# Kernel tuning notes

Hardware: AMD Instinct MI355X
Metric: run time of the kernel (lower is better)

The kernel has to match this reference:

```python
import jax, jax.numpy as jnp
import numpy as np

N_NODES = 50000
N_EDGES = 1600000
IN_DIM, HID, HEADS, OUT_DIM = 128, 32, 4, 16
NEG_SLOPE = 0.2  # DGL GATConv default


def setup_inputs() -> dict:
    key = jax.random.key(0)
    ks = jax.random.split(key, 12)
    features = jax.random.normal(ks[0], (N_NODES, IN_DIM), dtype=jnp.float32)
    src = jax.random.randint(ks[1], (N_EDGES,), 0, N_NODES, dtype=jnp.int32)
    dst = jax.random.randint(ks[2], (N_EDGES,), 0, N_NODES, dtype=jnp.int32)
    # layer 1 params (xavier-style scale)
    W1 = jax.random.normal(ks[3], (IN_DIM, HEADS * HID), dtype=jnp.float32) * (2.0 / (IN_DIM + HEADS * HID)) ** 0.5
    al1 = jax.random.normal(ks[4], (HEADS, HID), dtype=jnp.float32) * 0.1
    ar1 = jax.random.normal(ks[5], (HEADS, HID), dtype=jnp.float32) * 0.1
    b1 = jnp.zeros((HEADS * HID,), dtype=jnp.float32)
    # layer 2 params
    W2 = jax.random.normal(ks[6], (HID, OUT_DIM), dtype=jnp.float32) * (2.0 / (HID + OUT_DIM)) ** 0.5
    al2 = jax.random.normal(ks[7], (1, OUT_DIM), dtype=jnp.float32) * 0.1
    ar2 = jax.random.normal(ks[8], (1, OUT_DIM), dtype=jnp.float32) * 0.1
    b2 = jnp.zeros((OUT_DIM,), dtype=jnp.float32)
    return {"features": features, "src": src, "dst": dst,
            "W1": W1, "al1": al1, "ar1": ar1, "b1": b1,
            "W2": W2, "al2": al2, "ar2": ar2, "b2": b2}


def gat_conv(x, src, dst, W, al, ar, b, n_nodes):
    """DGL GATConv (no dropout, no residual). Returns [N, H, out]."""
    H, out = al.shape
    feat = (x @ W).reshape(-1, H, out)                       # [N,H,out]
    el = jnp.sum(feat * al, axis=-1)                         # [N,H]
    er = jnp.sum(feat * ar, axis=-1)                         # [N,H]
    e = jax.nn.leaky_relu(el[src] + er[dst], NEG_SLOPE)      # [E,H]
    # segment softmax over incoming edges per destination node
    m = jax.ops.segment_max(e, dst, num_segments=n_nodes)    # [N,H]
    ex = jnp.exp(e - m[dst])                                 # [E,H]
    s = jax.ops.segment_sum(ex, dst, num_segments=n_nodes)   # [N,H]
    alpha = ex / s[dst]                                      # [E,H]
    msg = alpha[:, :, None] * feat[src]                      # [E,H,out]
    rst = jax.ops.segment_sum(msg, dst, num_segments=n_nodes)
    return rst + b.reshape(H, out)


def reference(features, src, dst, W1, al1, ar1, b1, W2, al2, ar2, b2):
    n = features.shape[0]
    x1 = gat_conv(features, src, dst, W1, al1, ar1, b1, n)   # [N,HEADS,HID]
    x1 = jnp.mean(jax.nn.relu(x1), axis=1)                   # [N,HID]
    x2 = gat_conv(x1, src, dst, W2, al2, ar2, b2, n)         # [N,1,OUT]
    x2 = jnp.squeeze(x2, axis=1)                             # [N,OUT]
    return jax.nn.log_softmax(x2, axis=-1)
```

## Files before the change

### kernel.cpp

```cpp
#include <hip/hip_runtime.h>
#include <math.h>

#define NEG_SLOPE 0.2f
#define BINCAP 10240

typedef __attribute__((ext_vector_type(8))) short short8;
typedef __attribute__((ext_vector_type(4))) float f32x4;

__device__ __forceinline__ float lrelu(float x) {
    return x >= 0.f ? x : NEG_SLOPE * x;
}
__device__ __forceinline__ unsigned bf16_rne(float f) {
    unsigned b = __float_as_uint(f);
    return (b + 0x7FFFu + ((b >> 16) & 1u)) >> 16;
}

__global__ __launch_bounds__(256) void init_cursor(int* __restrict__ bin_cursor) {
    bin_cursor[threadIdx.x] = threadIdx.x * BINCAP;
}

__global__ __launch_bounds__(256) void scatter_bins(
    const int* __restrict__ src, const int* __restrict__ dst,
    int* __restrict__ bin_cursor, unsigned* __restrict__ binned,
    int E, int nbins)
{
    __shared__ int hist[256];
    __shared__ int base_l[256];
    int tid = threadIdx.x;
    hist[tid] = 0;
    __syncthreads();
    int epb = (E + gridDim.x - 1) / gridDim.x;
    int beg = blockIdx.x * epb, end = min(E, beg + epb);
    for (int e = beg + tid; e < end; e += 256)
        atomicAdd(&hist[dst[e] >> 8], 1);
    __syncthreads();
    if (tid < nbins) {
        int c = hist[tid];
        base_l[tid] = (c > 0) ? atomicAdd(&bin_cursor[tid], c) : 0;
    }
    __syncthreads();
    hist[tid] = 0;
    __syncthreads();
    for (int e = beg + tid; e < end; e += 256) {
        int d = dst[e];
        int bin = d >> 8;
        int slot = atomicAdd(&hist[bin], 1);
        binned[base_l[bin] + slot] = ((unsigned)(d & 255) << 16) | (unsigned)src[e];
    }
}

__global__ __launch_bounds__(256) void local_sort(
    const unsigned* __restrict__ binned, const int* __restrict__ bin_cursor,
    int* __restrict__ rowptr, unsigned short* __restrict__ deg,
    unsigned short* __restrict__ csr, int N, int nbins)
{
    __shared__ int cnt[256];
    __shared__ int sh[256];
    int b = blockIdx.x;
    int t = threadIdx.x;
    int gbase = b * BINCAP;
    int gcount = bin_cursor[b] - gbase;
    cnt[t] = 0;
    __syncthreads();
    for (int i = t; i < gcount; i += 256)
        atomicAdd(&cnt[binned[gbase + i] >> 16], 1);
    __syncthreads();
    int own = cnt[t];
    sh[t] = own;
    __syncthreads();
#pragma unroll
    for (int off = 1; off < 256; off <<= 1) {
        int v = (t >= off) ? sh[t - off] : 0;
        __syncthreads();
        sh[t] += v;
        __syncthreads();
    }
    int excl = sh[t] - own;
    int dcount = min(256, N - (b << 8));
    if (t < dcount) {
        rowptr[(b << 8) + t] = gbase + excl;
        deg[(b << 8) + t] = (unsigned short)own;
    }
    cnt[t] = excl;
    __syncthreads();
    for (int i = t; i < gcount; i += 256) {
        unsigned w = binned[gbase + i];
        int slot = atomicAdd(&cnt[w >> 16], 1);
        csr[gbase + slot] = (unsigned short)(w & 0xFFFFu);
    }
}

__global__ __launch_bounds__(256) void convert_w1(
    const float* __restrict__ W, unsigned short* __restrict__ Wt)
{
    int i = blockIdx.x * 256 + threadIdx.x;
    int kin = i >> 7, nout = i & 127;
    Wt[nout * 128 + kin] = (unsigned short)bf16_rne(W[kin * 128 + nout]);
}

__global__ __launch_bounds__(256) void gemm1_mfma(
    const float* __restrict__ X, const unsigned short* __restrict__ Wt,
    unsigned short* __restrict__ feat1b, int N)
{
    __shared__ unsigned short Xb[64][136];
    __shared__ unsigned short Wb[128][136];
    int tid = threadIdx.x;
    int nb = blockIdx.x * 64;

    for (int idx = tid; idx < 128 * 16; idx += 256) {
        int row = idx >> 4, q = idx & 15;
        *(uint4*)&Wb[row][q * 8] = *(const uint4*)&Wt[row * 128 + q * 8];
    }
    for (int idx = tid; idx < 64 * 32; idx += 256) {
        int row = idx >> 5, q = idx & 31;
        int n = nb + row;
        float4 v = (n < N) ? *(const float4*)&X[(size_t)n * 128 + q * 4]
                           : make_float4(0.f, 0.f, 0.f, 0.f);
        unsigned lo = bf16_rne(v.x) | (bf16_rne(v.y) << 16);
        unsigned hi = bf16_rne(v.z) | (bf16_rne(v.w) << 16);
        *(uint2*)&Xb[row][q * 4] = make_uint2(lo, hi);
    }
    __syncthreads();

    int wave = tid >> 6, lane = tid & 63;
    int m = lane & 15, quad = lane >> 4;
    f32x4 acc[8];
#pragma unroll
    for (int t = 0; t < 8; ++t) acc[t] = (f32x4){0.f, 0.f, 0.f, 0.f};

#pragma unroll
    for (int kt = 0; kt < 4; ++kt) {
        int k0 = kt * 32 + quad * 8;
        short8 a = *(const short8*)&Xb[wave * 16 + m][k0];
#pragma unroll
        for (int t = 0; t < 8; ++t) {
            short8 b = *(const short8*)&Wb[t * 16 + m][k0];
            acc[t] = __builtin_amdgcn_mfma_f32_16x16x32_bf16(a, b, acc[t], 0, 0, 0);
        }
    }

#pragma unroll
    for (int r = 0; r < 4; ++r) {
        int n = nb + wave * 16 + quad * 4 + r;
        if (n < N) {
#pragma unroll
            for (int t = 0; t < 8; ++t)
                feat1b[(size_t)n * 128 + t * 16 + m] =
                    (unsigned short)bf16_rne(acc[t][r]);
        }
    }
}

__global__ __launch_bounds__(256) void el_er1(
    const unsigned short* __restrict__ feat1b, const float* __restrict__ al,
    const float* __restrict__ ar, float* __restrict__ el1,
    float* __restrict__ er1, int N)
{
    int t = blockIdx.x * 256 + threadIdx.x;
    if (t >= N * 4) return;
    int n = t >> 2, h = t & 3;
    const unsigned* fp = (const unsigned*)(feat1b + (size_t)n * 128 + h * 32);
    const float* alh = al + h * 32;
    const float* arh = ar + h * 32;
    float pel = 0.f, per = 0.f;
#pragma unroll
    for (int q = 0; q < 16; ++q) {
        unsigned u = fp[q];
        float f0 = __uint_as_float(u << 16);
        float f1 = __uint_as_float(u & 0xFFFF0000u);
        pel += f0 * alh[2 * q] + f1 * alh[2 * q + 1];
        per += f0 * arh[2 * q] + f1 * arh[2 * q + 1];
    }
    el1[t] = pel;
    er1[t] = per;
}

__global__ __launch_bounds__(256) void agg1_fused(
    const int* __restrict__ rowptr, const unsigned short* __restrict__ deg,
    const unsigned short* __restrict__ csr,
    const unsigned short* __restrict__ feat1b, const float* __restrict__ el1,
    const float* __restrict__ er1, const float* __restrict__ b1,
    const float* __restrict__ W2, const float* __restrict__ al2,
    const float* __restrict__ ar2, unsigned short* __restrict__ feat2b,
    float* __restrict__ el2, float* __restrict__ er2, int N)
{
    __shared__ uint2 pairs[4][4][66];
    int gid = blockIdx.x * 256 + threadIdx.x;
    int d = gid >> 6;
    if (d >= N) return;
    int wv = (threadIdx.x >> 6) & 3;
    int lane = threadIdx.x & 63;
    int h = lane >> 4;
    float4 er4 = ((const float4*)er1)[d];
    int beg = rowptr[d], end = beg + (int)deg[d];
    const unsigned* feat32 = (const unsigned*)feat1b;

    float M = -INFINITY, S = 0.f, a0 = 0.f, a1 = 0.f;

    for (int base = beg; base < end; base += 64) {
        int cnt = min(64, end - base);
        int sn = 0;
        float4 v = make_float4(-INFINITY, -INFINITY, -INFINITY, -INFINITY);
        if (lane < cnt) {
            sn = (int)csr[base + lane];
            float4 el4 = ((const float4*)el1)[sn];
            v.x = lrelu(el4.x + er4.x);
            v.y = lrelu(el4.y + er4.y);
            v.z = lrelu(el4.z + er4.z);
            v.w = lrelu(el4.w + er4.w);
        }
        float4 cm = v;
#pragma unroll
        for (int off = 1; off < 64; off <<= 1) {
            cm.x = fmaxf(cm.x, __shfl_xor(cm.x, off));
            cm.y = fmaxf(cm.y, __shfl_xor(cm.y, off));
            cm.z = fmaxf(cm.z, __shfl_xor(cm.z, off));
            cm.w = fmaxf(cm.w, __shfl_xor(cm.w, off));
        }
        float4 w;
        w.x = __expf(v.x - cm.x);
        w.y = __expf(v.y - cm.y);
        w.z = __expf(v.z - cm.z);
        w.w = __expf(v.w - cm.w);
        unsigned snb = (unsigned)sn << 6;
        pairs[wv][0][lane] = make_uint2(snb, __float_as_uint(w.x));
        pairs[wv][1][lane] = make_uint2(snb, __float_as_uint(w.y));
        pairs[wv][2][lane] = make_uint2(snb, __float_as_uint(w.z));
        pairs[wv][3][lane] = make_uint2(snb, __float_as_uint(w.w));

        float cmh = (h & 2) ? ((h & 1) ? cm.w : cm.z) : ((h & 1) ? cm.y : cm.x);
        float nM = fmaxf(M, cmh);
        float so = __expf(M - nM);
        float sc = __expf(cmh - nM);
        M = nM;

        float ca0 = 0.f, ca1 = 0.f, cs = 0.f;
        for (int i = 0; i < cnt; ++i) {
            uint2 p = pairs[wv][h][i];
            float wb = __uint_as_float(p.y);
            unsigned u = feat32[p.x + lane];
            float f0 = __uint_as_float(u << 16);
            float f1 = __uint_as_float(u & 0xFFFF0000u);
            ca0 += wb * f0;
            ca1 += wb * f1;
            cs += wb;
        }
        S = S * so + cs * sc;
        a0 = a0 * so + ca0 * sc;
        a1 = a1 * so + ca1 * sc;
    }
    float inv = (end > beg) ? (1.f / S) : 0.f;
    float o0 = a0 * inv, o1 = a1 * inv;

    int dim0 = lane * 2;
    float2 bb = *(const float2*)(b1 + dim0);
    float r0 = fmaxf(o0 + bb.x, 0.f);
    float r1 = fmaxf(o1 + bb.y, 0.f);
    r0 += __shfl_xor(r0, 16); r0 += __shfl_xor(r0, 32);
    r1 += __shfl_xor(r1, 16); r1 += __shfl_xor(r1, 32);
    float u0 = 0.25f * r0;
    float u1 = 0.25f * r1;

    int j = lane & 15;
    float f2 = 0.f;
#pragma unroll
    for (int i = 0; i < 16; ++i) {
        float xa = __shfl(u0, i);
        float xb = __shfl(u1, i);
        f2 += xa * W2[(2 * i) * 16 + j] + xb * W2[(2 * i + 1) * 16 + j];
    }
    float pel = f2 * al2[j], per = f2 * ar2[j];
#pragma unroll
    for (int off = 1; off < 16; off <<= 1) {
        pel += __shfl_xor(pel, off);
        per += __shfl_xor(per, off);
    }
    if (lane < 16) feat2b[(size_t)d * 16 + j] = (unsigned short)bf16_rne(f2);
    if (lane == 0) { el2[d] = pel; er2[d] = per; }
}

__global__ __launch_bounds__(256) void agg2_fused(
    const int* __restrict__ rowptr, const unsigned short* __restrict__ deg,
    const unsigned short* __restrict__ csr,
    const unsigned short* __restrict__ feat2b, const float* __restrict__ el2,
    const float* __restrict__ er2, const float* __restrict__ b2,
    float* __restrict__ out, int N)
{
    __shared__ uint2 pairs2[4][4][18];
    int gid = blockIdx.x * 256 + threadIdx.x;
    int d = gid >> 4;
    if (d >= N) return;
    int tid = threadIdx.x;
    int wv = (tid >> 6) & 3;
    int grp = (tid >> 4) & 3;
    int l16 = tid & 15;
    float er = er2[d];
    int beg = rowptr[d], end = beg + (int)deg[d];

    float M = -INFINITY, S = 0.f, a = 0.f;
    for (int cb = beg; cb < end; cb += 16) {
        int cnt = min(16, end - cb);
        int sn = 0;
        float v = -INFINITY;
        if (l16 < cnt) {
            sn = (int)csr[cb + l16];
            v = lrelu(el2[sn] + er);
        }
        float cm = v;
#pragma unroll
        for (int off = 1; off < 16; off <<= 1)
            cm = fmaxf(cm, __shfl_xor(cm, off));
        float w = __expf(v - cm);
        pairs2[wv][grp][l16] = make_uint2((unsigned)sn << 4, __float_as_uint(w));
        float nM = fmaxf(M, cm);
        float so = __expf(M - nM);
        float sc = __expf(cm - nM);
        M = nM;
        float ca = 0.f, cs = 0.f;
        for (int i = 0; i < cnt; ++i) {
            uint2 p = pairs2[wv][grp][i];
            float wb = __uint_as_float(p.y);
            unsigned u = (unsigned)feat2b[p.x + l16];
            float f = __uint_as_float(u << 16);
            ca += wb * f;
            cs += wb;
        }
        S = S * so + cs * sc;
        a = a * so + ca * sc;
    }
    float inv = (end > beg) ? (1.f / S) : 0.f;
    float val = a * inv + b2[l16];
    float mm = val;
#pragma unroll
    for (int off = 1; off < 16; off <<= 1)
        mm = fmaxf(mm, __shfl_xor(mm, off));
    float ex = __expf(val - mm);
    float ssum = ex;
#pragma unroll
    for (int off = 1; off < 16; off <<= 1)
        ssum += __shfl_xor(ssum, off);
    out[(size_t)d * 16 + l16] = val - (mm + __logf(ssum));
}

extern "C" void kernel_launch(void* const* d_in, const int* in_sizes, int n_in,
                              void* d_out, int out_size, void* d_ws, size_t ws_size,
                              hipStream_t stream)
{
    const float* X   = (const float*)d_in[0];
    const int*   src = (const int*)d_in[1];
    const int*   dst = (const int*)d_in[2];
    const float* W1  = (const float*)d_in[3];
    const float* al1 = (const float*)d_in[4];
    const float* ar1 = (const float*)d_in[5];
    const float* b1  = (const float*)d_in[6];
    const float* W2  = (const float*)d_in[7];
    const float* al2 = (const float*)d_in[8];
    const float* ar2 = (const float*)d_in[9];
    const float* b2  = (const float*)d_in[10];
    int N = in_sizes[0] / 128;
    int E = in_sizes[1];
    int nbins = (N + 255) >> 8;

    float* ws = (float*)d_ws;
    size_t o = 0;
    unsigned short* feat1b = (unsigned short*)(ws + o); o += (size_t)N * 64;
    float* el1   = ws + o; o += (size_t)N * 4;
    float* er1   = ws + o; o += (size_t)N * 4;
    unsigned short* feat2b = (unsigned short*)(ws + o); o += (size_t)N * 8;
    float* el2   = ws + o; o += (size_t)N;
    float* er2   = ws + o; o += (size_t)N;
    int* rowptr  = (int*)(ws + o); o += (size_t)N;
    unsigned short* deg = (unsigned short*)(ws + o); o += (size_t)N / 2 + 1;
    unsigned short* Wt1b = (unsigned short*)(ws + o); o += 128 * 128 / 2;
    int* bin_cursor = (int*)(ws + o); o += 256;
    unsigned* binned = (unsigned*)(ws + o); o += (size_t)nbins * BINCAP;
    unsigned short* csr = (unsigned short*)(ws + o); o += (size_t)nbins * BINCAP / 2 + 1;
    float* out = (float*)d_out;

    init_cursor<<<1, 256, 0, stream>>>(bin_cursor);
    scatter_bins<<<256, 256, 0, stream>>>(src, dst, bin_cursor, binned, E, nbins);
    local_sort<<<nbins, 256, 0, stream>>>(binned, bin_cursor, rowptr, deg, csr, N, nbins);

    convert_w1<<<64, 256, 0, stream>>>(W1, Wt1b);
    gemm1_mfma<<<(N + 63) / 64, 256, 0, stream>>>(X, Wt1b, feat1b, N);
    el_er1<<<(N * 4 + 255) / 256, 256, 0, stream>>>(feat1b, al1, ar1, el1, er1, N);

    agg1_fused<<<(N * 64 + 255) / 256, 256, 0, stream>>>(
        rowptr, deg, csr, feat1b, el1, er1, b1, W2, al2, ar2, feat2b, el2, er2, N);

    agg2_fused<<<(N * 16 + 255) / 256, 256, 0, stream>>>(
        rowptr, deg, csr, feat2b, el2, er2, b2, out, N);
}
```

Before: 250.9 us.

## Fuse prep kernels, stage edges in LDS, fuse el/er into GEMM, widen agg2

Merges init_cursor and convert_w1 into a single prep launch, and fuses the el/er attention-logit computation into the MFMA GEMM epilogue using shuffle reductions, which removes a pass over feat1b. scatter_bins now runs with 512 blocks and stages packed (dst,src) words in shared memory, so dst and src are read from global memory only once. agg2 moves from 16 lanes per node to a full 64-lane wave that splits edges across four sub-groups and then reduces, and agg1's accumulators use float2 vectors. The trade-offs are more shared memory per scatter block, less precise el/er (computed from fp32 accumulators instead of rounded bf16), and wasted lanes in agg2 for low-degree nodes.

Result: no change. 251.0 us (+0.1%).

```diff
diff --git a/kernel.cpp b/kernel.cpp
--- a/kernel.cpp
+++ b/kernel.cpp
@@ -6,6 +6,7 @@
 
 typedef __attribute__((ext_vector_type(8))) short short8;
 typedef __attribute__((ext_vector_type(4))) float f32x4;
+typedef __attribute__((ext_vector_type(2))) float f32x2;
 
 __device__ __forceinline__ float lrelu(float x) {
     return x >= 0.f ? x : NEG_SLOPE * x;
@@ -15,8 +16,17 @@
     return (b + 0x7FFFu + ((b >> 16) & 1u)) >> 16;
 }
 
-__global__ __launch_bounds__(256) void init_cursor(int* __restrict__ bin_cursor) {
-    bin_cursor[threadIdx.x] = threadIdx.x * BINCAP;
+__global__ __launch_bounds__(256) void prep(
+    const float* __restrict__ W, unsigned short* __restrict__ Wt,
+    int* __restrict__ bin_cursor)
+{
+    if (blockIdx.x == 64) {
+        bin_cursor[threadIdx.x] = threadIdx.x * BINCAP;
+        return;
+    }
+    int i = blockIdx.x * 256 + threadIdx.x;
+    int kin = i >> 7, nout = i & 127;
+    Wt[nout * 128 + kin] = (unsigned short)bf16_rne(W[kin * 128 + nout]);
 }
 
 __global__ __launch_bounds__(256) void scatter_bins(
@@ -24,6 +34,7 @@
     int* __restrict__ bin_cursor, unsigned* __restrict__ binned,
     int E, int nbins)
 {
+    __shared__ unsigned stage[3328];
     __shared__ int hist[256];
     __shared__ int base_l[256];
     int tid = threadIdx.x;
@@ -31,8 +42,12 @@
     __syncthreads();
     int epb = (E + gridDim.x - 1) / gridDim.x;
     int beg = blockIdx.x * epb, end = min(E, beg + epb);
-    for (int e = beg + tid; e < end; e += 256)
-        atomicAdd(&hist[dst[e] >> 8], 1);
+    int cnt_local = end - beg;
+    for (int k = tid; k < cnt_local; k += 256) {
+        int d = dst[beg + k];
+        stage[k] = ((unsigned)d << 16) | (unsigned)src[beg + k];
+        atomicAdd(&hist[d >> 8], 1);
+    }
     __syncthreads();
     if (tid < nbins) {
         int c = hist[tid];
@@ -41,11 +56,11 @@
     __syncthreads();
     hist[tid] = 0;
     __syncthreads();
-    for (int e = beg + tid; e < end; e += 256) {
-        int d = dst[e];
-        int bin = d >> 8;
+    for (int k = tid; k < cnt_local; k += 256) {
+        unsigned w = stage[k];
+        int bin = w >> 24;
         int slot = atomicAdd(&hist[bin], 1);
-        binned[base_l[bin] + slot] = ((unsigned)(d & 255) << 16) | (unsigned)src[e];
+        binned[base_l[bin] + slot] = w;
     }
 }
 
@@ -63,7 +78,7 @@
     cnt[t] = 0;
     __syncthreads();
     for (int i = t; i < gcount; i += 256)
-        atomicAdd(&cnt[binned[gbase + i] >> 16], 1);
+        atomicAdd(&cnt[(binned[gbase + i] >> 16) & 255], 1);
     __syncthreads();
     int own = cnt[t];
     sh[t] = own;
@@ -85,22 +100,16 @@
     __syncthreads();
     for (int i = t; i < gcount; i += 256) {
         unsigned w = binned[gbase + i];
-        int slot = atomicAdd(&cnt[w >> 16], 1);
+        int slot = atomicAdd(&cnt[(w >> 16) & 255], 1);
         csr[gbase + slot] = (unsigned short)(w & 0xFFFFu);
     }
-}
-
-__global__ __launch_bounds__(256) void convert_w1(
-    const float* __restrict__ W, unsigned short* __restrict__ Wt)
-{
-    int i = blockIdx.x * 256 + threadIdx.x;
-    int kin = i >> 7, nout = i & 127;
-    Wt[nout * 128 + kin] = (unsigned short)bf16_rne(W[kin * 128 + nout]);
 }
 
 __global__ __launch_bounds__(256) void gemm1_mfma(
     const float* __restrict__ X, const unsigned short* __restrict__ Wt,
-    unsigned short* __restrict__ feat1b, int N)
+    const float* __restrict__ al, const float* __restrict__ ar,
+    unsigned short* __restrict__ feat1b, float* __restrict__ el1,
+    float* __restrict__ er1, int N)
 {
     __shared__ unsigned short Xb[64][136];
     __shared__ unsigned short Wb[128][136];
@@ -139,40 +148,45 @@
         }
     }
 
+    float al_lo[4], al_hi[4], ar_lo[4], ar_hi[4];
+#pragma unroll
+    for (int h = 0; h < 4; ++h) {
+        al_lo[h] = al[h * 32 + m];       al_hi[h] = al[h * 32 + 16 + m];
+        ar_lo[h] = ar[h * 32 + m];       ar_hi[h] = ar[h * 32 + 16 + m];
+    }
+
 #pragma unroll
     for (int r = 0; r < 4; ++r) {
         int n = nb + wave * 16 + quad * 4 + r;
+        float pel[4], per[4];
+#pragma unroll
+        for (int h = 0; h < 4; ++h) {
+            float fa = acc[2 * h][r], fb = acc[2 * h + 1][r];
+            pel[h] = fa * al_lo[h] + fb * al_hi[h];
+            per[h] = fa * ar_lo[h] + fb * ar_hi[h];
+        }
+#pragma unroll
+        for (int off = 1; off < 16; off <<= 1) {
+#pragma unroll
+            for (int h = 0; h < 4; ++h) {
+                pel[h] += __shfl_xor(pel[h], off);
+                per[h] += __shfl_xor(per[h], off);
+            }
+        }
         if (n < N) {
 #pragma unroll
             for (int t = 0; t < 8; ++t)
                 feat1b[(size_t)n * 128 + t * 16 + m] =
                     (unsigned short)bf16_rne(acc[t][r]);
-        }
-    }
-}
-
-__global__ __launch_bounds__(256) void el_er1(
-    const unsigned short* __restrict__ feat1b, const float* __restrict__ al,
-    const float* __restrict__ ar, float* __restrict__ el1,
-    float* __restrict__ er1, int N)
-{
-    int t = blockIdx.x * 256 + threadIdx.x;
-    if (t >= N * 4) return;
-    int n = t >> 2, h = t & 3;
-    const unsigned* fp = (const unsigned*)(feat1b + (size_t)n * 128 + h * 32);
-    const float* alh = al + h * 32;
-    const float* arh = ar + h * 32;
-    float pel = 0.f, per = 0.f;
-#pragma unroll
-    for (int q = 0; q < 16; ++q) {
-        unsigned u = fp[q];
-        float f0 = __uint_as_float(u << 16);
-        float f1 = __uint_as_float(u & 0xFFFF0000u);
-        pel += f0 * alh[2 * q] + f1 * alh[2 * q + 1];
-        per += f0 * arh[2 * q] + f1 * arh[2 * q + 1];
-    }
-    el1[t] = pel;
-    er1[t] = per;
+            if (m == 0) {
+#pragma unroll
+                for (int h = 0; h < 4; ++h) {
+                    el1[(size_t)n * 4 + h] = pel[h];
+                    er1[(size_t)n * 4 + h] = per[h];
+                }
+            }
+        }
+    }
 }
 
 __global__ __launch_bounds__(256) void agg1_fused(
@@ -195,7 +209,8 @@
     int beg = rowptr[d], end = beg + (int)deg[d];
     const unsigned* feat32 = (const unsigned*)feat1b;
 
-    float M = -INFINITY, S = 0.f, a0 = 0.f, a1 = 0.f;
+    float M = -INFINITY, S = 0.f;
+    f32x2 A = {0.f, 0.f};
 
     for (int base = beg; base < end; base += 64) {
         int cnt = min(64, end - base);
@@ -234,23 +249,22 @@
         float sc = __expf(cmh - nM);
         M = nM;
 
-        float ca0 = 0.f, ca1 = 0.f, cs = 0.f;
+        f32x2 ca = {0.f, 0.f};
+        float cs = 0.f;
         for (int i = 0; i < cnt; ++i) {
             uint2 p = pairs[wv][h][i];
             float wb = __uint_as_float(p.y);
             unsigned u = feat32[p.x + lane];
-            float f0 = __uint_as_float(u << 16);
-            float f1 = __uint_as_float(u & 0xFFFF0000u);
-            ca0 += wb * f0;
-            ca1 += wb * f1;
+            f32x2 f = {__uint_as_float(u << 16),
+                       __uint_as_float(u & 0xFFFF0000u)};
+            ca += (f32x2){wb, wb} * f;
             cs += wb;
         }
         S = S * so + cs * sc;
-        a0 = a0 * so + ca0 * sc;
-        a1 = a1 * so + ca1 * sc;
+        A = A * (f32x2){so, so} + ca * (f32x2){sc, sc};
     }
     float inv = (end > beg) ? (1.f / S) : 0.f;
-    float o0 = a0 * inv, o1 = a1 * inv;
+    float o0 = A.x * inv, o1 = A.y * inv;
 
     int dim0 = lane * 2;
     float2 bb = *(const float2*)(b1 + dim0);
@@ -286,50 +300,54 @@
     const float* __restrict__ er2, const float* __restrict__ b2,
     float* __restrict__ out, int N)
 {
-    __shared__ uint2 pairs2[4][4][18];
+    __shared__ uint2 pairs2[4][64];
     int gid = blockIdx.x * 256 + threadIdx.x;
-    int d = gid >> 4;
+    int d = gid >> 6;
     if (d >= N) return;
-    int tid = threadIdx.x;
-    int wv = (tid >> 6) & 3;
-    int grp = (tid >> 4) & 3;
-    int l16 = tid & 15;
+    int wv = (threadIdx.x >> 6) & 3;
+    int lane = threadIdx.x & 63;
+    int sub = lane >> 4, dim = lane & 15;
     float er = er2[d];
     int beg = rowptr[d], end = beg + (int)deg[d];
 
     float M = -INFINITY, S = 0.f, a = 0.f;
-    for (int cb = beg; cb < end; cb += 16) {
-        int cnt = min(16, end - cb);
+    for (int cb = beg; cb < end; cb += 64) {
+        int cnt = min(64, end - cb);
         int sn = 0;
         float v = -INFINITY;
-        if (l16 < cnt) {
-            sn = (int)csr[cb + l16];
+        if (lane < cnt) {
+            sn = (int)csr[cb + lane];
             v = lrelu(el2[sn] + er);
         }
         float cm = v;
 #pragma unroll
-        for (int off = 1; off < 16; off <<= 1)
+        for (int off = 1; off < 64; off <<= 1)
             cm = fmaxf(cm, __shfl_xor(cm, off));
         float w = __expf(v - cm);
-        pairs2[wv][grp][l16] = make_uint2((unsigned)sn << 4, __float_as_uint(w));
+        float cs = w;
+#pragma unroll
+        for (int off = 1; off < 64; off <<= 1)
+            cs += __shfl_xor(cs, off);
+        pairs2[wv][lane] = make_uint2((unsigned)sn << 4, __float_as_uint(w));
+
         float nM = fmaxf(M, cm);
         float so = __expf(M - nM);
         float sc = __expf(cm - nM);
         M = nM;
-        float ca = 0.f, cs = 0.f;
-        for (int i = 0; i < cnt; ++i) {
-            uint2 p = pairs2[wv][grp][i];
+        float ca = 0.f;
+        for (int i = sub; i < cnt; i += 4) {
+            uint2 p = pairs2[wv][i];
             float wb = __uint_as_float(p.y);
-            unsigned u = (unsigned)feat2b[p.x + l16];
-            float f = __uint_as_float(u << 16);
-            ca += wb * f;
-            cs += wb;
+            unsigned u = (unsigned)feat2b[p.x + dim];
+            ca += wb * __uint_as_float(u << 16);
         }
         S = S * so + cs * sc;
         a = a * so + ca * sc;
     }
+    a += __shfl_xor(a, 16);
+    a += __shfl_xor(a, 32);
     float inv = (end > beg) ? (1.f / S) : 0.f;
-    float val = a * inv + b2[l16];
+    float val = a * inv + b2[dim];
     float mm = val;
 #pragma unroll
     for (int off = 1; off < 16; off <<= 1)
@@ -339,7 +357,8 @@
 #pragma unroll
     for (int off = 1; off < 16; off <<= 1)
         ssum += __shfl_xor(ssum, off);
-    out[(size_t)d * 16 + l16] = val - (mm + __logf(ssum));
+    if (lane < 16)
+        out[(size_t)d * 16 + dim] = val - (mm + __logf(ssum));
 }
 
 extern "C" void kernel_launch(void* const* d_in, const int* in_sizes, int n_in,
@@ -377,17 +396,15 @@
     unsigned short* csr = (unsigned short*)(ws + o); o += (size_t)nbins * BINCAP / 2 + 1;
     float* out = (float*)d_out;
 
-    init_cursor<<<1, 256, 0, stream>>>(bin_cursor);
-    scatter_bins<<<256, 256, 0, stream>>>(src, dst, bin_cursor, binned, E, nbins);
+    prep<<<65, 256, 0, stream>>>(W1, Wt1b, bin_cursor);
+    scatter_bins<<<512, 256, 0, stream>>>(src, dst, bin_cursor, binned, E, nbins);
     local_sort<<<nbins, 256, 0, stream>>>(binned, bin_cursor, rowptr, deg, csr, N, nbins);
 
-    convert_w1<<<64, 256, 0, stream>>>(W1, Wt1b);
-    gemm1_mfma<<<(N + 63) / 64, 256, 0, stream>>>(X, Wt1b, feat1b, N);
-    el_er1<<<(N * 4 + 255) / 256, 256, 0, stream>>>(feat1b, al1, ar1, el1, er1, N);
+    gemm1_mfma<<<(N + 63) / 64, 256, 0, stream>>>(X, Wt1b, al1, ar1, feat1b, el1, er1, N);
 
     agg1_fused<<<(N * 64 + 255) / 256, 256, 0, stream>>>(
         rowptr, deg, csr, feat1b, el1, er1, b1, W2, al2, ar2, feat2b, el2, er2, N);
 
-    agg2_fused<<<(N * 16 + 255) / 256, 256, 0, stream>>>(
+    agg2_fused<<<(N * 64 + 255) / 256, 256, 0, stream>>>(
         rowptr, deg, csr, feat2b, el2, er2, b2, out, N);
 }
```
